# Kernel optimization log

Measured on AMD Instinct MI355X. Metric: run time of the kernel, lower is better.

The kernel has to match this reference:

```python
import jax, jax.numpy as jnp
import numpy as np

NUM_HEADS = 16
NEG = -1e9

def setup_inputs() -> dict:
    key = jax.random.key(0)
    ks = jax.random.split(key, 5)
    B, S, D = 4, 2048, 1024
    scale = 1.0 / np.sqrt(D)
    return {
        "x": jax.random.normal(ks[0], (B, S, D), dtype=jnp.float32),
        "WQ": jax.random.normal(ks[1], (D, D), dtype=jnp.float32) * scale,
        "WK": jax.random.normal(ks[2], (D, D), dtype=jnp.float32) * scale,
        "WV": jax.random.normal(ks[3], (D, D), dtype=jnp.float32) * scale,
        "WO": jax.random.normal(ks[4], (D, D), dtype=jnp.float32) * scale,
    }

def _split_heads(t, h):
    # [..., s, h*d] -> [..., h, s, d]
    *lead, s, hd = t.shape
    return jnp.swapaxes(t.reshape(*lead, s, h, hd // h), -3, -2)

def reference(x, WQ, WK, WV, WO):
    h = NUM_HEADS
    S = x.shape[-2]
    # Linear stores weight [out, in]; y = x @ W^T
    Q = _split_heads(x @ WQ.T, h)  # [b,h,s,dk]
    K = _split_heads(x @ WK.T, h)
    V = _split_heads(x @ WV.T, h)
    dk = Q.shape[-1]
    scores = jnp.einsum('bhqd,bhkd->bhqk', Q, K) / jnp.sqrt(jnp.float32(dk))
    causal = jnp.tril(jnp.ones((S, S), dtype=bool))  # allowed positions
    scores = jnp.where(causal, scores, NEG)
    # explicit stable softmax (matches source)
    m = jnp.max(scores, axis=-1, keepdims=True)
    e = jnp.exp(scores - m)
    attn = e / jnp.sum(e, axis=-1, keepdims=True)
    out = jnp.einsum('bhqk,bhkd->bhqd', attn, V)  # [b,h,s,dv]
    out = jnp.swapaxes(out, -3, -2).reshape(*x.shape[:-1], -1)  # [b,s,h*dv]
    return out @ WO.T
```

## Files before the change

kernel.cpp:

```cpp
#include <hip/hip_runtime.h>
#include <stdint.h>
#include <math.h>

typedef __attribute__((ext_vector_type(8))) short bf16x8;
typedef __attribute__((ext_vector_type(4))) short v4s;
typedef __attribute__((ext_vector_type(4))) float f32x4;
typedef __attribute__((ext_vector_type(4))) unsigned short u16x4;
typedef __attribute__((ext_vector_type(2))) unsigned int u32x2;

#define MFMA16(a,b,c)   __builtin_amdgcn_mfma_f32_16x16x32_bf16((a),(b),(c),0,0,0)
#define MFMA16K(a,b,c)  __builtin_amdgcn_mfma_f32_16x16x16bf16_1k((a),(b),(c),0,0,0)

static __device__ __forceinline__ void gld_lds16(const void* g, void* l) {
  __builtin_amdgcn_global_load_lds(
      (const __attribute__((address_space(1))) unsigned int*)g,
      (__attribute__((address_space(3))) unsigned int*)l,
      16, 0, 0);
}

static __device__ __forceinline__ unsigned short f2bf(float f) {
  unsigned int u = __builtin_bit_cast(unsigned int, f);
  return (unsigned short)((u + 0x8000u) >> 16);
}

__global__ __launch_bounds__(256) void cvt_kernel(const float* __restrict__ in,
                                                  unsigned short* __restrict__ out,
                                                  int n4) {
  int i = blockIdx.x * blockDim.x + threadIdx.x;
  int stride = gridDim.x * blockDim.x;
  for (; i < n4; i += stride) {
    float4 v = ((const float4*)in)[i];
    u16x4 o;
    o.x = f2bf(v.x); o.y = f2bf(v.y); o.z = f2bf(v.z); o.w = f2bf(v.w);
    ((u16x4*)out)[i] = o;
  }
}

__global__ __launch_bounds__(256) void cvt4_kernel(const float* __restrict__ w0,
                                                   const float* __restrict__ w1,
                                                   const float* __restrict__ w2,
                                                   const float* __restrict__ w3,
                                                   unsigned short* __restrict__ out) {
  const float* in = (blockIdx.y == 0) ? w0 : (blockIdx.y == 1) ? w1
                  : (blockIdx.y == 2) ? w2 : w3;
  unsigned short* o = out + (size_t)blockIdx.y * 1048576;
  int i = blockIdx.x * blockDim.x + threadIdx.x;
  int stride = gridDim.x * blockDim.x;
  for (; i < 1048576/4; i += stride) {
    float4 v = ((const float4*)in)[i];
    u16x4 t;
    t.x = f2bf(v.x); t.y = f2bf(v.y); t.z = f2bf(v.z); t.w = f2bf(v.w);
    ((u16x4*)o)[i] = t;
  }
}

template<int MODE, typename CT>
__device__ __forceinline__ void gemm_bt_tile(const unsigned short* __restrict__ A,
                                             const unsigned short* __restrict__ Bt,
                                             CT* __restrict__ C,
                                             int m0, int n0,
                                             unsigned short* As,
                                             unsigned short* Bs)
{
  const int tid  = threadIdx.x;
  const int w    = tid >> 6, lane = tid & 63;
  const int quad = lane >> 4, c0 = lane & 15;
  const int wm   = w >> 1, wn = w & 1;

  const unsigned short* ga[2];
  const unsigned short* gb[2];
  int ldsoff[2];
  #pragma unroll
  for (int i = 0; i < 2; ++i) {
    int f = i*4096 + w*1024 + lane*16;
    int r = f >> 6;
    int q = (f >> 4) & 3;
    ga[i] = A  + (m0 + r)*1024 + q*8;
    gb[i] = Bt + (n0 + r)*1024 + q*8;
    ldsoff[i] = i*4096 + w*1024;
  }

  int aAddr[4], bAddr[4];
  #pragma unroll
  for (int t = 0; t < 4; ++t) {
    aAddr[t] = (wm*64 + t*16 + c0)*64 + quad*16;
    bAddr[t] = (wn*64 + t*16 + c0)*64 + quad*16;
  }

  f32x4 acc[4][4];
  #pragma unroll
  for (int i = 0; i < 4; ++i)
    #pragma unroll
    for (int j = 0; j < 4; ++j)
      acc[i][j] = (f32x4){0.f, 0.f, 0.f, 0.f};

  for (int kt = 0; kt < 32; ++kt) {
    __syncthreads();
    #pragma unroll
    for (int i = 0; i < 2; ++i) {
      gld_lds16(ga[i] + kt*32, (char*)As + ldsoff[i]);
      gld_lds16(gb[i] + kt*32, (char*)Bs + ldsoff[i]);
    }
    __syncthreads();

    bf16x8 af[4], bfr[4];
    #pragma unroll
    for (int t = 0; t < 4; ++t) af[t]  = *(const bf16x8*)((const char*)As + aAddr[t]);
    #pragma unroll
    for (int t = 0; t < 4; ++t) bfr[t] = *(const bf16x8*)((const char*)Bs + bAddr[t]);

    #pragma unroll
    for (int mt = 0; mt < 4; ++mt)
      #pragma unroll
      for (int nt = 0; nt < 4; ++nt)
        acc[mt][nt] = MFMA16(af[mt], bfr[nt], acc[mt][nt]);
  }

  const float scl = (MODE == 3) ? 0.1803368801f : 1.0f;
  #pragma unroll
  for (int mt = 0; mt < 4; ++mt) {
    #pragma unroll
    for (int nt = 0; nt < 4; ++nt) {
      if (MODE == 2) {
        u16x4 pk;
        #pragma unroll
        for (int r = 0; r < 4; ++r) pk[r] = f2bf(acc[mt][nt][r]);
        int s0 = m0 + wm*64 + mt*16 + quad*4;
        int gc = n0 + wn*64 + nt*16 + c0;
        int b = s0 >> 11, ss = s0 & 2047;
        int h = gc >> 6, d = gc & 63;
        *(u16x4*)((unsigned short*)C + (size_t)(((b << 4) + h)*64 + d)*2048 + ss) = pk;
      } else {
        #pragma unroll
        for (int r = 0; r < 4; ++r) {
          int gr = m0 + wm*64 + mt*16 + quad*4 + r;
          int gc = n0 + wn*64 + nt*16 + c0;
          if (MODE == 0 || MODE == 3) {
            int b = gr >> 11, s = gr & 2047;
            int h = gc >> 6, d = gc & 63;
            ((unsigned short*)C)[(((b << 4) + h)*2048 + s)*64 + d] = f2bf(acc[mt][nt][r] * scl);
          } else {
            ((float*)C)[gr*1024 + gc] = acc[mt][nt][r];
          }
        }
      }
    }
  }
}

__global__ __launch_bounds__(256) void qkv_kernel(
    const unsigned short* __restrict__ X,
    const unsigned short* __restrict__ WQ, const unsigned short* __restrict__ WK,
    const unsigned short* __restrict__ WV,
    unsigned short* __restrict__ Q, unsigned short* __restrict__ K,
    unsigned short* __restrict__ V)
{
  __shared__ __align__(16) unsigned short As[128*32];
  __shared__ __align__(16) unsigned short Bs[128*32];
  if (blockIdx.z == 2) {
    gemm_bt_tile<2>(X, WV, V, blockIdx.x*128, blockIdx.y*128, As, Bs);
  } else if (blockIdx.z == 0) {
    gemm_bt_tile<3>(X, WQ, Q, blockIdx.x*128, blockIdx.y*128, As, Bs);
  } else {
    gemm_bt_tile<0>(X, WK, K, blockIdx.x*128, blockIdx.y*128, As, Bs);
  }
}

__global__ __launch_bounds__(256) void proj_kernel(
    const unsigned short* __restrict__ A,
    const unsigned short* __restrict__ WO,
    float* __restrict__ C)
{
  __shared__ __align__(16) unsigned short As[128*32];
  __shared__ __align__(16) unsigned short Bs[128*32];
  gemm_bt_tile<1>(A, WO, C, blockIdx.x*128, blockIdx.y*128, As, Bs);
}

__global__ __launch_bounds__(256, 2) void attn_kernel(
    const unsigned short* __restrict__ Q,
    const unsigned short* __restrict__ K,
    const unsigned short* __restrict__ Vt,
    unsigned short* __restrict__ O)
{
  __shared__ __align__(16) unsigned short VtL[2][64*128];
  __shared__ __align__(16) unsigned short KL[2][128*64];

  const int tid  = threadIdx.x;
  const int w    = tid >> 6, lane = tid & 63;
  const int quad = lane >> 4, c0 = lane & 15;
  const int bx = blockIdx.y, bh = blockIdx.x;

  const unsigned short* Qh = Q  + (size_t)bh*2048*64;
  const unsigned short* Kh = K  + (size_t)bh*2048*64;
  const unsigned short* Vh = Vt + (size_t)bh*64*2048;

  const unsigned short* vga[4];
  const unsigned short* kga[4];
  int ldso[4];
  #pragma unroll
  for (int i = 0; i < 4; ++i) {
    int cid = i*256 + tid;
    int vr = cid >> 4, vq = cid & 15;
    vga[i] = Vh + (size_t)vr*2048 + (vq ^ (vr & 15))*8;
    int kr = cid >> 3, kq = cid & 7;
    kga[i] = Kh + (size_t)kr*64 + (kq ^ (kr & 7))*8;
    ldso[i] = i*4096 + w*1024;
  }

  const int b = bh >> 4, h = bh & 15;

  #define ATTN_MK_BODY(mk, Kb, Vb, DIAG)                                          \
  {                                                                               \
    bf16x8 ka0 = *(const bf16x8*)((const char*)(Kb) + ((mk)*16 + c0)*128          \
                                  + (((0*4 + quad) ^ (c0 & 7)) * 16));            \
    bf16x8 ka1 = *(const bf16x8*)((const char*)(Kb) + ((mk)*16 + c0)*128          \
                                  + (((1*4 + quad) ^ (c0 & 7)) * 16));            \
    f32x4 s0 = (f32x4){0.f,0.f,0.f,0.f}, s1 = (f32x4){0.f,0.f,0.f,0.f};           \
    s0 = MFMA16(ka0, qf[0][0], s0);                                               \
    s1 = MFMA16(ka0, qf[1][0], s1);                                               \
    s0 = MFMA16(ka1, qf[0][1], s0);                                               \
    s1 = MFMA16(ka1, qf[1][1], s1);                                               \
    if (DIAG) {                                                                   \
      _Pragma("unroll")                                                           \
      for (int r = 0; r < 4; ++r) {                                               \
        int kk = (mk)*16 + quad*4 + r;                                            \
        if (kk > w*32 + c0)      s0[r] = -1e30f;                                  \
        if (kk > w*32 + 16 + c0) s1[r] = -1e30f;                                  \
      }                                                                           \
    }                                                                             \
    float p00 = __builtin_amdgcn_exp2f(s0[0]), p01 = __builtin_amdgcn_exp2f(s0[1]); \
    float p02 = __builtin_amdgcn_exp2f(s0[2]), p03 = __builtin_amdgcn_exp2f(s0[3]); \
    float p10 = __builtin_amdgcn_exp2f(s1[0]), p11 = __builtin_amdgcn_exp2f(s1[1]); \
    float p12 = __builtin_amdgcn_exp2f(s1[2]), p13 = __builtin_amdgcn_exp2f(s1[3]); \
    l_r[0] += (p00 + p01) + (p02 + p03);                                          \
    l_r[1] += (p10 + p11) + (p12 + p13);                                          \
    u32x2 a0, a1;                                                                 \
    a0.x = __builtin_amdgcn_perm(__builtin_bit_cast(unsigned int, p01),           \
                                 __builtin_bit_cast(unsigned int, p00), 0x07060302u); \
    a0.y = __builtin_amdgcn_perm(__builtin_bit_cast(unsigned int, p03),           \
                                 __builtin_bit_cast(unsigned int, p02), 0x07060302u); \
    a1.x = __builtin_amdgcn_perm(__builtin_bit_cast(unsigned int, p11),           \
                                 __builtin_bit_cast(unsigned int, p10), 0x07060302u); \
    a1.y = __builtin_amdgcn_perm(__builtin_bit_cast(unsigned int, p13),           \
                                 __builtin_bit_cast(unsigned int, p12), 0x07060302u); \
    v4s pa0 = __builtin_bit_cast(v4s, a0);                                        \
    v4s pa1 = __builtin_bit_cast(v4s, a1);                                        \
    _Pragma("unroll")                                                             \
    for (int dt = 0; dt < 4; ++dt) {                                              \
      int vr = dt*16 + c0;                                                        \
      int p  = 2*(mk) + (quad >> 1);                                              \
      v4s vb = *(const v4s*)((const char*)(Vb) + vr*256 + ((p ^ c0) * 16) + (quad & 1)*8); \
      o_[0][dt] = MFMA16K(pa0, vb, o_[0][dt]);                                    \
      o_[1][dt] = MFMA16K(pa1, vb, o_[1][dt]);                                    \
    }                                                                             \
  }

  for (int pi = 0; pi < 2; ++pi) {
    const int qt = pi ? bx : 15 - bx;

    bf16x8 qf[2][2];
    #pragma unroll
    for (int mq = 0; mq < 2; ++mq)
      #pragma unroll
      for (int ks = 0; ks < 2; ++ks)
        qf[mq][ks] = *(const bf16x8*)(Qh + (qt*128 + w*32 + mq*16 + c0)*64 + ks*32 + quad*8);

    f32x4 o_[2][4];
    float l_r[2] = {0.f, 0.f};
    #pragma unroll
    for (int mq = 0; mq < 2; ++mq)
      #pragma unroll
      for (int dt = 0; dt < 4; ++dt) o_[mq][dt] = (f32x4){0.f, 0.f, 0.f, 0.f};

    __syncthreads();
    #pragma unroll
    for (int i = 0; i < 4; ++i) {
      gld_lds16(vga[i], (char*)VtL[0] + ldso[i]);
      gld_lds16(kga[i], (char*)KL[0]  + ldso[i]);
    }

    for (int kt = 0; kt < qt; ++kt) {
      __syncthreads();
      #pragma unroll
      for (int i = 0; i < 4; ++i) {
        gld_lds16(vga[i] + (kt+1)*128,  (char*)VtL[(kt+1)&1] + ldso[i]);
        gld_lds16(kga[i] + (kt+1)*8192, (char*)KL[(kt+1)&1]  + ldso[i]);
      }
      const unsigned short* Vb = VtL[kt & 1];
      const unsigned short* Kb = KL[kt & 1];
      __builtin_amdgcn_s_setprio(1);
      #pragma unroll
      for (int mk = 0; mk < 8; ++mk)
        ATTN_MK_BODY(mk, Kb, Vb, false)
      __builtin_amdgcn_s_setprio(0);
    }

    {
      __syncthreads();
      const unsigned short* Vb = VtL[qt & 1];
      const unsigned short* Kb = KL[qt & 1];
      __builtin_amdgcn_s_setprio(1);
      #pragma unroll
      for (int mk = 0; mk < 8; ++mk)
        if (mk < 2*w + 2)
          ATTN_MK_BODY(mk, Kb, Vb, true)
      __builtin_amdgcn_s_setprio(0);
    }

    #pragma unroll
    for (int mq = 0; mq < 2; ++mq) {
      l_r[mq] += __shfl_xor(l_r[mq], 16);
      l_r[mq] += __shfl_xor(l_r[mq], 32);
    }
    #pragma unroll
    for (int mt = 0; mt < 2; ++mt) {
      #pragma unroll
      for (int r = 0; r < 4; ++r) {
        float l = __shfl(l_r[mt], quad*4 + r);
        float inv = 1.0f / l;
        int srow = qt*128 + w*32 + mt*16 + quad*4 + r;
        #pragma unroll
        for (int dt = 0; dt < 4; ++dt) {
          int col = h*64 + dt*16 + c0;
          O[((size_t)b*2048 + srow)*1024 + col] = f2bf(o_[mt][dt][r] * inv);
        }
      }
    }
  }
  #undef ATTN_MK_BODY
}

extern "C" void kernel_launch(void* const* d_in, const int* in_sizes, int n_in,
                              void* d_out, int out_size, void* d_ws, size_t ws_size,
                              hipStream_t stream) {
  const float* xf  = (const float*)d_in[0];
  const float* wqf = (const float*)d_in[1];
  const float* wkf = (const float*)d_in[2];
  const float* wvf = (const float*)d_in[3];
  const float* wof = (const float*)d_in[4];
  float* out = (float*)d_out;
  unsigned short* ws = (unsigned short*)d_ws;

  const bool fused = ws_size >= (size_t)58720256;

  if (fused) {
    unsigned short* xb  = ws;
    unsigned short* wb  = ws + 8388608;
    unsigned short* Kw  = ws + 12582912;
    unsigned short* Vw  = ws + 20971520;
    unsigned short* Ow  = xb;
    unsigned short* Qd  = (unsigned short*)out;

    cvt_kernel <<<2048, 256, 0, stream>>>(xf, xb, 8388608/4);
    cvt4_kernel<<<dim3(256, 4), 256, 0, stream>>>(wqf, wkf, wvf, wof, wb);

    qkv_kernel <<<dim3(64, 8, 3), 256, 0, stream>>>(xb, wb, wb + 1048576, wb + 2097152,
                                                    Qd, Kw, Vw);
    attn_kernel<<<dim3(64, 8),    256, 0, stream>>>(Qd, Kw, Vw, Ow);
    proj_kernel<<<dim3(64, 8),    256, 0, stream>>>(Ow, wb + 3145728, out);
  } else {
    unsigned short* xb  = ws;
    unsigned short* wb  = ws + 8388608;
    unsigned short* Kw  = ws + 12582912;
    unsigned short* Vw  = ws + 14680064;
    unsigned short* Ow  = ws + 16777216;

    cvt_kernel <<<2048, 256, 0, stream>>>(xf, xb, 8388608/4);
    cvt4_kernel<<<dim3(256, 4), 256, 0, stream>>>(wqf, wkf, wvf, wof, wb);

    for (int b = 0; b < 4; ++b) {
      const unsigned short* xbb = xb  + (size_t)b * 2048 * 1024;
      float*               outb = out + (size_t)b * 2048 * 1024;
      unsigned short*        Qd = (unsigned short*)outb;
      qkv_kernel <<<dim3(16, 8, 3), 256, 0, stream>>>(xbb, wb, wb + 1048576, wb + 2097152,
                                                      Qd, Kw, Vw);
      attn_kernel<<<dim3(16, 8),    256, 0, stream>>>(Qd, Kw, Vw, Ow);
      proj_kernel<<<dim3(16, 8),    256, 0, stream>>>(Ow, wb + 3145728, outb);
    }
  }
}
```

Baseline: 238.7 us.

## Double-buffer GEMM LDS tiles and widen K step to 64

The QKV and output-projection GEMM tile now uses a K step of 64 instead of 32 and ping-pongs between two LDS buffers. The next tile's global-to-LDS load is issued right after the barrier, so it overlaps with the MFMAs on the current buffer, and the number of barriers per tile is halved. LDS use per block grows fourfold (64KB total), which can lower occupancy, and the 128-byte row stride may cause LDS bank conflicts on the fragment reads.

```diff
diff --git a/kernel.cpp b/kernel.cpp
--- a/kernel.cpp
+++ b/kernel.cpp
@@ -67,14 +67,14 @@
   const int quad = lane >> 4, c0 = lane & 15;
   const int wm   = w >> 1, wn = w & 1;
 
-  const unsigned short* ga[2];
-  const unsigned short* gb[2];
-  int ldsoff[2];
-  #pragma unroll
-  for (int i = 0; i < 2; ++i) {
-    int f = i*4096 + w*1024 + lane*16;
-    int r = f >> 6;
-    int q = (f >> 4) & 3;
+  const unsigned short* ga[4];
+  const unsigned short* gb[4];
+  int ldsoff[4];
+  #pragma unroll
+  for (int i = 0; i < 4; ++i) {
+    int cid = i*256 + tid;
+    int r = cid >> 3;
+    int q = cid & 7;
     ga[i] = A  + (m0 + r)*1024 + q*8;
     gb[i] = Bt + (n0 + r)*1024 + q*8;
     ldsoff[i] = i*4096 + w*1024;
@@ -83,8 +83,8 @@
   int aAddr[4], bAddr[4];
   #pragma unroll
   for (int t = 0; t < 4; ++t) {
-    aAddr[t] = (wm*64 + t*16 + c0)*64 + quad*16;
-    bAddr[t] = (wn*64 + t*16 + c0)*64 + quad*16;
+    aAddr[t] = (wm*64 + t*16 + c0)*128 + quad*16;
+    bAddr[t] = (wn*64 + t*16 + c0)*128 + quad*16;
   }
 
   f32x4 acc[4][4];
@@ -94,27 +94,44 @@
     for (int j = 0; j < 4; ++j)
       acc[i][j] = (f32x4){0.f, 0.f, 0.f, 0.f};
 
-  for (int kt = 0; kt < 32; ++kt) {
-    __syncthreads();
-    #pragma unroll
-    for (int i = 0; i < 2; ++i) {
-      gld_lds16(ga[i] + kt*32, (char*)As + ldsoff[i]);
-      gld_lds16(gb[i] + kt*32, (char*)Bs + ldsoff[i]);
-    }
-    __syncthreads();
-
-    bf16x8 af[4], bfr[4];
-    #pragma unroll
-    for (int t = 0; t < 4; ++t) af[t]  = *(const bf16x8*)((const char*)As + aAddr[t]);
-    #pragma unroll
-    for (int t = 0; t < 4; ++t) bfr[t] = *(const bf16x8*)((const char*)Bs + bAddr[t]);
-
-    #pragma unroll
-    for (int mt = 0; mt < 4; ++mt)
-      #pragma unroll
-      for (int nt = 0; nt < 4; ++nt)
-        acc[mt][nt] = MFMA16(af[mt], bfr[nt], acc[mt][nt]);
-  }
+  #pragma unroll
+  for (int i = 0; i < 4; ++i) {
+    gld_lds16(ga[i], (char*)As + ldsoff[i]);
+    gld_lds16(gb[i], (char*)Bs + ldsoff[i]);
+  }
+
+  #define GEMM_STEP(kt, CB, NB, LAST)                                             \
+  {                                                                               \
+    __syncthreads();                   \
+    if (!(LAST)) {                                                                \
+      _Pragma("unroll")                                                           \
+      for (int i = 0; i < 4; ++i) {                                               \
+        gld_lds16(ga[i] + ((kt)+1)*64, (char*)As + (NB) + ldsoff[i]);             \
+        gld_lds16(gb[i] + ((kt)+1)*64, (char*)Bs + (NB) + ldsoff[i]);             \
+      }                                                                           \
+    }                                                                             \
+    _Pragma("unroll")                                                             \
+    for (int kk = 0; kk < 2; ++kk) {                                              \
+      bf16x8 af[4], bfr[4];                                                       \
+      _Pragma("unroll")                                                           \
+      for (int t = 0; t < 4; ++t)                                                 \
+        af[t]  = *(const bf16x8*)((const char*)As + (CB) + aAddr[t] + kk*64);     \
+      _Pragma("unroll")                                                           \
+      for (int t = 0; t < 4; ++t)                                                 \
+        bfr[t] = *(const bf16x8*)((const char*)Bs + (CB) + bAddr[t] + kk*64);     \
+      _Pragma("unroll")                                                           \
+      for (int mt = 0; mt < 4; ++mt)                                              \
+        _Pragma("unroll")                                                         \
+        for (int nt = 0; nt < 4; ++nt)                                            \
+          acc[mt][nt] = MFMA16(af[mt], bfr[nt], acc[mt][nt]);                     \
+    }                                                                             \
+  }
+
+  for (int it = 0; it < 8; ++it) {
+    GEMM_STEP(2*it,     0, 16384, false)
+    GEMM_STEP(2*it+1, 16384,   0, (it == 7))
+  }
+  #undef GEMM_STEP
 
   const float scl = (MODE == 3) ? 0.1803368801f : 1.0f;
   #pragma unroll
@@ -155,8 +172,8 @@
     unsigned short* __restrict__ Q, unsigned short* __restrict__ K,
     unsigned short* __restrict__ V)
 {
-  __shared__ __align__(16) unsigned short As[128*32];
-  __shared__ __align__(16) unsigned short Bs[128*32];
+  __shared__ __align__(16) unsigned short As[2*128*64];
+  __shared__ __align__(16) unsigned short Bs[2*128*64];
   if (blockIdx.z == 2) {
     gemm_bt_tile<2>(X, WV, V, blockIdx.x*128, blockIdx.y*128, As, Bs);
   } else if (blockIdx.z == 0) {
@@ -171,8 +188,8 @@
     const unsigned short* __restrict__ WO,
     float* __restrict__ C)
 {
-  __shared__ __align__(16) unsigned short As[128*32];
-  __shared__ __align__(16) unsigned short Bs[128*32];
+  __shared__ __align__(16) unsigned short As[2*128*64];
+  __shared__ __align__(16) unsigned short Bs[2*128*64];
   gemm_bt_tile<1>(A, WO, C, blockIdx.x*128, blockIdx.y*128, As, Bs);
 }
 
```

Result: no change. 241.0 us (+1.0%).
